# Optimization experiments

Hardware: AMD Instinct MI355X
Metric: run time of the kernel (lower is better)

## Reference

```python
import jax, jax.numpy as jnp
import numpy as np

NEG_BIG = -2.0**32 + 1.0

def setup_inputs() -> dict:
    key = jax.random.key(0)
    ks = jax.random.split(key, 8)
    B, T, D = 4096, 200, 32
    H1, H2 = 80, 40
    s = lambda n: 1.0 / np.sqrt(n)
    return {
        "q": jax.random.normal(ks[0], (B, D), jnp.float32),
        "k": jax.random.normal(ks[1], (B, T, D), jnp.float32),
        "v": jax.random.normal(ks[2], (B, T, D), jnp.float32),
        "mask": jax.random.randint(ks[3], (B, T), 0, 2, jnp.int32),
        "Wq": jax.random.normal(ks[4], (D, D), jnp.float32) * s(D),
        "bq": jnp.zeros((D,), jnp.float32),
        "alpha": jnp.zeros((D,), jnp.float32),  # Keras PReLU default alpha=0
        "W1": jax.random.normal(ks[5], (4 * D, H1), jnp.float32) * s(4 * D),
        "b1": jnp.zeros((H1,), jnp.float32),
        "W2": jax.random.normal(ks[6], (H1, H2), jnp.float32) * s(H1),
        "b2": jnp.zeros((H2,), jnp.float32),
        "Wf": jax.random.normal(ks[7], (H2, 1), jnp.float32) * s(H2),
        "bf": jnp.zeros((1,), jnp.float32),
    }

def prelu(x, a):
    return jnp.where(x >= 0, x, a * x)

def reference(q, k, v, mask, Wq, bq, alpha, W1, b1, W2, b2, Wf, bf):
    # dense_q with PReLU activation: [B, D] -> [B, 32]
    qp = prelu(q @ Wq + bq, alpha)
    # tile query across history steps: [B, T, 32]
    qt = jnp.broadcast_to(qp[:, None, :], k.shape)
    # DIN attention features: [B, T, 4*32]
    info = jnp.concatenate([qt, k, qt - k, qt * k], axis=-1)
    info = jax.nn.sigmoid(info @ W1 + b1)
    info = jax.nn.sigmoid(info @ W2 + b2)
    logits = (info @ Wf + bf).squeeze(-1)  # [B, T]
    logits = jnp.where(mask == 0, jnp.full_like(logits, NEG_BIG), logits)
    att = jax.nn.softmax(logits, axis=-1)
    return att[:, None, :]  # [B, 1, T]
```

## Files before the change

### kernel.cpp

```cpp
#include <hip/hip_runtime.h>
#include <math.h>

typedef float f32x4 __attribute__((ext_vector_type(4)));
typedef _Float16 f16;
typedef f16 f16x8 __attribute__((ext_vector_type(8)));
typedef unsigned int u32;
typedef u32 u32x2 __attribute__((ext_vector_type(2)));

#define BB 4096
#define TT 200
#define DD 32
#define H1 80
#define H2 40
#define SLAB_W 104
#define LOG2E 1.44269504f

__device__ __align__(16) float g_wqt[DD * DD];
__device__ __align__(16) float g_act[H1 * DD];
__device__ __align__(16) float g_bcf[5 * 64 * 8];
__device__ __align__(16) float g_df [5 * 64 * 8];
__device__ __align__(16) f16   g_w2h[9 * 64 * 8];

__device__ __forceinline__ float exp2_raw(float x) {
    float r;
    asm("v_exp_f32 %0, %1" : "=v"(r) : "v"(x));
    return r;
}
__device__ __forceinline__ float sig_pre(float a) {
    return __builtin_amdgcn_rcpf(1.f + exp2_raw(a));
}

__global__ void pack_kernel(const float* __restrict__ W1, const float* __restrict__ W2,
                            const float* __restrict__ Wq) {
    int idx = blockIdx.x * 256 + threadIdx.x;
    if (idx < DD * DD) {
        int col = idx / DD, e = idx % DD;
        g_wqt[idx] = Wq[e * DD + col];
        return;
    }
    idx -= DD * DD;
    if (idx < H1 * DD) {
        int c = idx / DD, d = idx % DD;
        g_act[idx] = -LOG2E * (W1[d * H1 + c] + W1[(64 + d) * H1 + c]);
        return;
    }
    idx -= H1 * DD;
    if (idx < 5 * 64 * 8) {
        int e = idx & 7, l = (idx >> 3) & 63, n = idx >> 9;
        int kidx = (l >> 4) * 8 + e;
        int j = n * 16 + (l & 15);
        g_bcf[idx] = -LOG2E * (W1[(32 + kidx) * H1 + j] - W1[(64 + kidx) * H1 + j]);
        g_df [idx] = -LOG2E * W1[(96 + kidx) * H1 + j];
        return;
    }
    idx -= 5 * 64 * 8;
    if (idx < 9 * 64 * 8) {
        int e = idx & 7, l = (idx >> 3) & 63, g = idx >> 9;
        int kt = g / 3, n = g % 3;
        int j   = kt * 32 + (l >> 4) * 8 + e;
        int col = n * 16 + (l & 15);
        float v = (j < H1 && col < H2) ? W2[j * H2 + col] : 0.f;
        g_w2h[idx] = (f16)(-LOG2E * v);
    }
}

__global__ __launch_bounds__(256) void din_mfma(
    const float* __restrict__ q, const float* __restrict__ k, const int* __restrict__ mask,
    const float* __restrict__ bq, const float* __restrict__ alpha,
    const float* __restrict__ b1, const float* __restrict__ b2, const float* __restrict__ Wf,
    float* __restrict__ out)
{
    const int tid = threadIdx.x;
    const int wid = tid >> 6, l = tid & 63;
    const int l15 = l & 15, lg4 = l >> 4;
    const int b   = (blockIdx.x << 2) | wid;

    __shared__ __align__(16) f16   slab[4][16][SLAB_W];
    __shared__ __align__(16) float u_s[4][H1];
    __shared__ __align__(16) float lgt[4][208];
    float* qp = lgt[wid];

    f16x8 W2r[9];
    #pragma unroll
    for (int g = 0; g < 9; ++g) W2r[g] = *(const f16x8*)(g_w2h + (g * 64 + l) * 8);

    const int* mrow = mask + (size_t)b * TT;
    int mk0 = mrow[l];
    int mk1 = mrow[64 + l];
    int mk2 = mrow[128 + l];
    int mk3 = (l < 8) ? mrow[192 + l] : 1;

    if (l < DD) {
        const f32x4* qv = (const f32x4*)(q + (size_t)b * DD);
        const f32x4* wv = (const f32x4*)(g_wqt + l * DD);
        float acc = bq[l];
        #pragma unroll
        for (int i = 0; i < 8; ++i) {
            f32x4 a = qv[i], w = wv[i];
            acc += (a[0] * w[0] + a[1] * w[1]) + (a[2] * w[2] + a[3] * w[3]);
        }
        float al = alpha[l];
        qp[l] = acc >= 0.f ? acc : al * acc;
    }
    {
        u32* z0 = (u32*)slab[wid];
        #pragma unroll
        for (int i = 0; i < 2; ++i) {
            int idx = i * 64 + l;
            z0[(idx >> 3) * 52 + 40 + (idx & 7)] = 0u;
        }
    }

    f32x4 qp4[8];
    #pragma unroll
    for (int j = 0; j < 8; ++j) qp4[j] = *(const f32x4*)(&qp[j * 4]);
    f32x4 qpa = *(const f32x4*)(&qp[lg4 * 8]);
    f32x4 qpb = *(const f32x4*)(&qp[lg4 * 8 + 4]);

    #pragma unroll
    for (int i = 0; i < 2; ++i) {
        int c = i * 64 + l;
        if (c < H1) {
            const f32x4* av = (const f32x4*)(g_act + c * DD);
            float acc = -LOG2E * b1[c];
            #pragma unroll
            for (int j = 0; j < 8; ++j) {
                f32x4 a = av[j], p = qp4[j];
                acc += (a[0] * p[0] + a[1] * p[1]) + (a[2] * p[2] + a[3] * p[3]);
            }
            u_s[wid][c] = acc;
        }
    }
    f16x8 Bh[5];
    #pragma unroll
    for (int n = 0; n < 5; ++n) {
        const f32x4* bv = (const f32x4*)(g_bcf + (n * 64 + l) * 8);
        const f32x4* dv = (const f32x4*)(g_df  + (n * 64 + l) * 8);
        f32x4 b0 = bv[0], b1v = bv[1], d0 = dv[0], d1 = dv[1];
        #pragma unroll
        for (int e = 0; e < 4; ++e) {
            Bh[n][e]     = (f16)(b0[e]  + qpa[e] * d0[e]);
            Bh[n][e + 4] = (f16)(b1v[e] + qpb[e] * d1[e]);
        }
    }
    f32x4 b2r[3], wfr[3];
    #pragma unroll
    for (int n = 0; n < 3; ++n) {
        int c0 = n * 16 + lg4 * 4;
        if (c0 + 3 < H2) {
            f32x4 bv = *(const f32x4*)(b2 + c0);
            f32x4 wv = *(const f32x4*)(Wf + c0);
            #pragma unroll
            for (int e = 0; e < 4; ++e) { bv[e] *= -LOG2E; wv[e] *= LOG2E; }
            b2r[n] = bv;
            wfr[n] = wv;
        } else {
            b2r[n] = (f32x4){0.f, 0.f, 0.f, 0.f};
            wfr[n] = (f32x4){0.f, 0.f, 0.f, 0.f};
        }
    }
    f32x4 ur[5];
    #pragma unroll
    for (int n = 0; n < 5; ++n) ur[n] = *(const f32x4*)(&u_s[wid][n * 16 + lg4 * 4]);

    const float* kb = k + (size_t)b * (TT * DD);
    f16 (*ws)[SLAB_W] = slab[wid];
    float* lg = lgt[wid];

    f32x4 x0, x1;
    auto loadk = [&](int m) {
        int t = m * 16 + l15; if (t > TT - 1) t = TT - 1;
        const f32x4* kr = (const f32x4*)(kb + t * DD + lg4 * 8);
        x0 = kr[0]; x1 = kr[1];
    };

    auto l1_full = [&](int nload) {
        f16x8 Ah;
        #pragma unroll
        for (int e = 0; e < 4; ++e) {
            Ah[e]     = (f16)x0[e];
            Ah[e + 4] = (f16)x1[e];
        }
        if (nload >= 0) loadk(nload);
        #pragma unroll
        for (int n = 0; n < 5; ++n) {
            int j0 = n * 16 + lg4 * 4;
            f32x4 acc = ur[n];
            acc = __builtin_amdgcn_mfma_f32_16x16x32_f16(Bh[n], Ah, acc, 0, 0, 0);
            auto p01 = __builtin_amdgcn_cvt_pkrtz(sig_pre(acc[0]), sig_pre(acc[1]));
            auto p23 = __builtin_amdgcn_cvt_pkrtz(sig_pre(acc[2]), sig_pre(acc[3]));
            u32x2 w;
            w[0] = __builtin_bit_cast(u32, p01);
            w[1] = __builtin_bit_cast(u32, p23);
            *(u32x2*)(&ws[l15][j0]) = w;
        }
    };

    auto body = [&](int m) {
        f16x8 sh0 = *(const f16x8*)(&ws[l15][0 * 32 + lg4 * 8]);
        f16x8 sh1 = *(const f16x8*)(&ws[l15][1 * 32 + lg4 * 8]);
        f16x8 sh2 = *(const f16x8*)(&ws[l15][2 * 32 + lg4 * 8]);

        if (m < 12) l1_full(m < 11 ? m + 2 : -1);

        f32x4 a0 = {0.f,0.f,0.f,0.f}, a1 = {0.f,0.f,0.f,0.f}, a2 = {0.f,0.f,0.f,0.f};
        #pragma unroll
        for (int kt = 0; kt < 3; ++kt) {
            f16x8 sh = (kt == 0) ? sh0 : (kt == 1) ? sh1 : sh2;
            a0 = __builtin_amdgcn_mfma_f32_16x16x32_f16(W2r[kt * 3 + 0], sh, a0, 0, 0, 0);
            a1 = __builtin_amdgcn_mfma_f32_16x16x32_f16(W2r[kt * 3 + 1], sh, a1, 0, 0, 0);
            a2 = __builtin_amdgcn_mfma_f32_16x16x32_f16(W2r[kt * 3 + 2], sh, a2, 0, 0, 0);
        }

        float pn[3];
        #pragma unroll
        for (int n = 0; n < 3; ++n) {
            f32x4 av = (n == 0) ? a0 : (n == 1) ? a1 : a2;
            float t0 = wfr[n][0] * sig_pre(av[0] + b2r[n][0]);
            float t1 = wfr[n][1] * sig_pre(av[1] + b2r[n][1]);
            float t2 = wfr[n][2] * sig_pre(av[2] + b2r[n][2]);
            float t3 = wfr[n][3] * sig_pre(av[3] + b2r[n][3]);
            pn[n] = (t0 + t1) + (t2 + t3);
        }
        float p = (pn[0] + pn[1]) + pn[2];
        p += __shfl_xor(p, 16);
        p += __shfl_xor(p, 32);
        if (l < 16) lg[m * 16 + l15] = p;
    };

    loadk(0);
    l1_full(1);
    for (int m = 0; m < 13; ++m) body(m);

    const float NEG = -4294967295.0f;
    float v0 = lg[l];        if (mk0 == 0) v0 = NEG;
    float v1 = lg[64 + l];   if (mk1 == 0) v1 = NEG;
    float v2 = lg[128 + l];  if (mk2 == 0) v2 = NEG;
    float v3 = -8589934590.0f;
    if (l < 8) { v3 = lg[192 + l]; if (mk3 == 0) v3 = NEG; }

    float mx = fmaxf(fmaxf(v0, v1), fmaxf(v2, v3));
    #pragma unroll
    for (int off = 32; off; off >>= 1) mx = fmaxf(mx, __shfl_xor(mx, off));

    float e0 = exp2_raw(v0 - mx), e1 = exp2_raw(v1 - mx);
    float e2 = exp2_raw(v2 - mx), e3 = exp2_raw(v3 - mx);
    float ssum = (e0 + e1) + (e2 + e3);
    #pragma unroll
    for (int off = 32; off; off >>= 1) ssum += __shfl_xor(ssum, off);

    float* orow = out + (size_t)b * TT;
    orow[l]       = e0 / ssum;
    orow[64 + l]  = e1 / ssum;
    orow[128 + l] = e2 / ssum;
    if (l < 8) orow[192 + l] = e3 / ssum;
}

extern "C" void kernel_launch(void* const* d_in, const int* in_sizes, int n_in,
                              void* d_out, int out_size, void* d_ws, size_t ws_size,
                              hipStream_t stream) {
    const float* q     = (const float*)d_in[0];
    const float* k     = (const float*)d_in[1];
    const int*   mask  = (const int*)d_in[3];
    const float* Wq    = (const float*)d_in[4];
    const float* bq    = (const float*)d_in[5];
    const float* alpha = (const float*)d_in[6];
    const float* W1    = (const float*)d_in[7];
    const float* b1    = (const float*)d_in[8];
    const float* W2    = (const float*)d_in[9];
    const float* b2    = (const float*)d_in[10];
    const float* Wf    = (const float*)d_in[11];
    float* out = (float*)d_out;

    hipLaunchKernelGGL(pack_kernel, dim3(52), dim3(256), 0, stream, W1, W2, Wq);
    hipLaunchKernelGGL(din_mfma, dim3(BB / 4), dim3(256), 0, stream,
                       q, k, mask, bq, alpha, b1, b2, Wf, out);
}
```

Baseline: 51.00 us.

## Split each batch row across two waves interleaving time tiles

```diff
diff --git a/kernel.cpp b/kernel.cpp
--- a/kernel.cpp
+++ b/kernel.cpp
@@ -73,24 +73,20 @@
     const int tid = threadIdx.x;
     const int wid = tid >> 6, l = tid & 63;
     const int l15 = l & 15, lg4 = l >> 4;
-    const int b   = (blockIdx.x << 2) | wid;
+    const int r   = wid >> 1, s = wid & 1;
+    const int b   = (blockIdx.x << 1) | r;
 
     __shared__ __align__(16) f16   slab[4][16][SLAB_W];
-    __shared__ __align__(16) float u_s[4][H1];
-    __shared__ __align__(16) float lgt[4][208];
-    float* qp = lgt[wid];
-
-    f16x8 W2r[9];
-    #pragma unroll
-    for (int g = 0; g < 9; ++g) W2r[g] = *(const f16x8*)(g_w2h + (g * 64 + l) * 8);
-
-    const int* mrow = mask + (size_t)b * TT;
-    int mk0 = mrow[l];
-    int mk1 = mrow[64 + l];
-    int mk2 = mrow[128 + l];
-    int mk3 = (l < 8) ? mrow[192 + l] : 1;
-
-    if (l < DD) {
+    __shared__ __align__(16) float qp_s[2][DD];
+    __shared__ __align__(16) float u_s[2][H1];
+    __shared__ __align__(16) float b2t[48], wft[48];
+    __shared__ __align__(16) float lgt[2][208];
+
+    if (tid < 48) {
+        b2t[tid] = tid < H2 ? -LOG2E * b2[tid] : 0.f;
+        wft[tid] = tid < H2 ? LOG2E * Wf[tid] : 0.f;
+    }
+    if (s == 0 && l < DD) {
         const f32x4* qv = (const f32x4*)(q + (size_t)b * DD);
         const f32x4* wv = (const f32x4*)(g_wqt + l * DD);
         float acc = bq[l];
@@ -100,7 +96,7 @@
             acc += (a[0] * w[0] + a[1] * w[1]) + (a[2] * w[2] + a[3] * w[3]);
         }
         float al = alpha[l];
-        qp[l] = acc >= 0.f ? acc : al * acc;
+        qp_s[r][l] = acc >= 0.f ? acc : al * acc;
     }
     {
         u32* z0 = (u32*)slab[wid];
@@ -111,11 +107,11 @@
         }
     }
 
+    __syncthreads();
+
     f32x4 qp4[8];
     #pragma unroll
-    for (int j = 0; j < 8; ++j) qp4[j] = *(const f32x4*)(&qp[j * 4]);
-    f32x4 qpa = *(const f32x4*)(&qp[lg4 * 8]);
-    f32x4 qpb = *(const f32x4*)(&qp[lg4 * 8 + 4]);
+    for (int j = 0; j < 8; ++j) qp4[j] = *(const f32x4*)(&qp_s[r][j * 4]);
 
     #pragma unroll
     for (int i = 0; i < 2; ++i) {
@@ -128,9 +124,11 @@
                 f32x4 a = av[j], p = qp4[j];
                 acc += (a[0] * p[0] + a[1] * p[1]) + (a[2] * p[2] + a[3] * p[3]);
             }
-            u_s[wid][c] = acc;
-        }
-    }
+            u_s[r][c] = acc;
+        }
+    }
+    f32x4 qpa = *(const f32x4*)(&qp_s[r][lg4 * 8]);
+    f32x4 qpb = *(const f32x4*)(&qp_s[r][lg4 * 8 + 4]);
     f16x8 Bh[5];
     #pragma unroll
     for (int n = 0; n < 5; ++n) {
@@ -143,49 +141,25 @@
             Bh[n][e + 4] = (f16)(b1v[e] + qpb[e] * d1[e]);
         }
     }
-    f32x4 b2r[3], wfr[3];
-    #pragma unroll
-    for (int n = 0; n < 3; ++n) {
-        int c0 = n * 16 + lg4 * 4;
-        if (c0 + 3 < H2) {
-            f32x4 bv = *(const f32x4*)(b2 + c0);
-            f32x4 wv = *(const f32x4*)(Wf + c0);
-            #pragma unroll
-            for (int e = 0; e < 4; ++e) { bv[e] *= -LOG2E; wv[e] *= LOG2E; }
-            b2r[n] = bv;
-            wfr[n] = wv;
-        } else {
-            b2r[n] = (f32x4){0.f, 0.f, 0.f, 0.f};
-            wfr[n] = (f32x4){0.f, 0.f, 0.f, 0.f};
-        }
-    }
-    f32x4 ur[5];
-    #pragma unroll
-    for (int n = 0; n < 5; ++n) ur[n] = *(const f32x4*)(&u_s[wid][n * 16 + lg4 * 4]);
 
     const float* kb = k + (size_t)b * (TT * DD);
     f16 (*ws)[SLAB_W] = slab[wid];
-    float* lg = lgt[wid];
-
-    f32x4 x0, x1;
-    auto loadk = [&](int m) {
+    float* lg = lgt[r];
+
+    auto l1 = [&](int m) {
         int t = m * 16 + l15; if (t > TT - 1) t = TT - 1;
         const f32x4* kr = (const f32x4*)(kb + t * DD + lg4 * 8);
-        x0 = kr[0]; x1 = kr[1];
-    };
-
-    auto l1_full = [&](int nload) {
+        f32x4 x0 = kr[0], x1 = kr[1];
         f16x8 Ah;
         #pragma unroll
         for (int e = 0; e < 4; ++e) {
             Ah[e]     = (f16)x0[e];
             Ah[e + 4] = (f16)x1[e];
         }
-        if (nload >= 0) loadk(nload);
         #pragma unroll
         for (int n = 0; n < 5; ++n) {
             int j0 = n * 16 + lg4 * 4;
-            f32x4 acc = ur[n];
+            f32x4 acc = *(const f32x4*)(&u_s[r][j0]);
             acc = __builtin_amdgcn_mfma_f32_16x16x32_f16(Bh[n], Ah, acc, 0, 0, 0);
             auto p01 = __builtin_amdgcn_cvt_pkrtz(sig_pre(acc[0]), sig_pre(acc[1]));
             auto p23 = __builtin_amdgcn_cvt_pkrtz(sig_pre(acc[2]), sig_pre(acc[3]));
@@ -197,40 +171,46 @@
     };
 
     auto body = [&](int m) {
-        f16x8 sh0 = *(const f16x8*)(&ws[l15][0 * 32 + lg4 * 8]);
-        f16x8 sh1 = *(const f16x8*)(&ws[l15][1 * 32 + lg4 * 8]);
-        f16x8 sh2 = *(const f16x8*)(&ws[l15][2 * 32 + lg4 * 8]);
-
-        if (m < 12) l1_full(m < 11 ? m + 2 : -1);
-
         f32x4 a0 = {0.f,0.f,0.f,0.f}, a1 = {0.f,0.f,0.f,0.f}, a2 = {0.f,0.f,0.f,0.f};
         #pragma unroll
         for (int kt = 0; kt < 3; ++kt) {
-            f16x8 sh = (kt == 0) ? sh0 : (kt == 1) ? sh1 : sh2;
-            a0 = __builtin_amdgcn_mfma_f32_16x16x32_f16(W2r[kt * 3 + 0], sh, a0, 0, 0, 0);
-            a1 = __builtin_amdgcn_mfma_f32_16x16x32_f16(W2r[kt * 3 + 1], sh, a1, 0, 0, 0);
-            a2 = __builtin_amdgcn_mfma_f32_16x16x32_f16(W2r[kt * 3 + 2], sh, a2, 0, 0, 0);
-        }
-
+            f16x8 sh = *(const f16x8*)(&ws[l15][kt * 32 + lg4 * 8]);
+            f16x8 w0 = *(const f16x8*)(g_w2h + ((kt * 3 + 0) * 64 + l) * 8);
+            f16x8 w1 = *(const f16x8*)(g_w2h + ((kt * 3 + 1) * 64 + l) * 8);
+            f16x8 w2 = *(const f16x8*)(g_w2h + ((kt * 3 + 2) * 64 + l) * 8);
+            a0 = __builtin_amdgcn_mfma_f32_16x16x32_f16(w0, sh, a0, 0, 0, 0);
+            a1 = __builtin_amdgcn_mfma_f32_16x16x32_f16(w1, sh, a1, 0, 0, 0);
+            a2 = __builtin_amdgcn_mfma_f32_16x16x32_f16(w2, sh, a2, 0, 0, 0);
+        }
         float pn[3];
         #pragma unroll
         for (int n = 0; n < 3; ++n) {
             f32x4 av = (n == 0) ? a0 : (n == 1) ? a1 : a2;
-            float t0 = wfr[n][0] * sig_pre(av[0] + b2r[n][0]);
-            float t1 = wfr[n][1] * sig_pre(av[1] + b2r[n][1]);
-            float t2 = wfr[n][2] * sig_pre(av[2] + b2r[n][2]);
-            float t3 = wfr[n][3] * sig_pre(av[3] + b2r[n][3]);
+            f32x4 bqv = *(const f32x4*)(&b2t[n * 16 + lg4 * 4]);
+            f32x4 wqv = *(const f32x4*)(&wft[n * 16 + lg4 * 4]);
+            float t0 = wqv[0] * sig_pre(av[0] + bqv[0]);
+            float t1 = wqv[1] * sig_pre(av[1] + bqv[1]);
+            float t2 = wqv[2] * sig_pre(av[2] + bqv[2]);
+            float t3 = wqv[3] * sig_pre(av[3] + bqv[3]);
             pn[n] = (t0 + t1) + (t2 + t3);
         }
         float p = (pn[0] + pn[1]) + pn[2];
         p += __shfl_xor(p, 16);
         p += __shfl_xor(p, 32);
         if (l < 16) lg[m * 16 + l15] = p;
+        if (m + 2 < 13) l1(m + 2);
     };
 
-    loadk(0);
-    l1_full(1);
-    for (int m = 0; m < 13; ++m) body(m);
+    l1(s);
+    for (int m = s; m < 13; m += 2) body(m);
+
+    const int* mrow = mask + (size_t)b * TT;
+    int mk0 = mrow[l];
+    int mk1 = mrow[64 + l];
+    int mk2 = mrow[128 + l];
+    int mk3 = (l < 8) ? mrow[192 + l] : 1;
+
+    __syncthreads();
 
     const float NEG = -4294967295.0f;
     float v0 = lg[l];        if (mk0 == 0) v0 = NEG;
@@ -250,10 +230,13 @@
     for (int off = 32; off; off >>= 1) ssum += __shfl_xor(ssum, off);
 
     float* orow = out + (size_t)b * TT;
-    orow[l]       = e0 / ssum;
-    orow[64 + l]  = e1 / ssum;
-    orow[128 + l] = e2 / ssum;
-    if (l < 8) orow[192 + l] = e3 / ssum;
+    if (s == 0) {
+        orow[l]      = e0 / ssum;
+        orow[64 + l] = e1 / ssum;
+    } else {
+        orow[128 + l] = e2 / ssum;
+        if (l < 8) orow[192 + l] = e3 / ssum;
+    }
 }
 
 extern "C" void kernel_launch(void* const* d_in, const int* in_sizes, int n_in,
@@ -273,6 +256,6 @@
     float* out = (float*)d_out;
 
     hipLaunchKernelGGL(pack_kernel, dim3(52), dim3(256), 0, stream, W1, W2, Wq);
-    hipLaunchKernelGGL(din_mfma, dim3(BB / 4), dim3(256), 0, stream,
+    hipLaunchKernelGGL(din_mfma, dim3(BB / 2), dim3(256), 0, stream,
                        q, k, mask, bq, alpha, b1, b2, Wf, out);
 }
```

Result: slower. 60.89 us (+19.4%).
